# Optimization experiments

Measured on AMD Instinct MI355X. Metric: run time of the kernel, lower is better.

The kernel has to match this reference:

```python
import jax, jax.numpy as jnp
import numpy as np
import math

D_MODEL = 1024
D_STATE = 16
D_CONV = 4
EXPAND = 2
D_INNER = D_MODEL * EXPAND
BATCH = 2
SEQ = 2048


def setup_inputs() -> dict:
    key = jax.random.key(0)
    ks = jax.random.split(key, 8)
    s = 0.02
    x = jax.random.normal(ks[0], (BATCH, SEQ, D_MODEL), dtype=jnp.float32)
    in_proj_w = jax.random.normal(ks[1], (D_MODEL, 2 * D_INNER), dtype=jnp.float32) * s
    conv_w = jax.random.normal(ks[2], (D_INNER, D_CONV), dtype=jnp.float32) * s
    conv_b = jnp.zeros((D_INNER,), dtype=jnp.float32)
    x_proj_w = jax.random.normal(ks[3], (D_INNER, 2 * D_STATE + 1), dtype=jnp.float32) * s
    A_log = jnp.log(jnp.broadcast_to(jnp.arange(1, D_STATE + 1, dtype=jnp.float32)[None, :], (D_INNER, D_STATE)))
    dt_w = jax.random.normal(ks[4], (D_INNER, 1), dtype=jnp.float32) * s
    # special dt bias init: softplus^{-1}(dt_init)
    u = jax.random.uniform(ks[5], (D_INNER,), dtype=jnp.float32)
    dt_init = jnp.exp(u * (math.log(0.1) - math.log(0.001)) + math.log(0.001))
    dt_b = dt_init + jnp.log(-jnp.expm1(-dt_init))
    out_proj_w = jax.random.normal(ks[6], (D_INNER, D_MODEL), dtype=jnp.float32) * s
    ln_g = jnp.ones((D_MODEL,), dtype=jnp.float32)
    ln_b = jnp.zeros((D_MODEL,), dtype=jnp.float32)
    return {"x": x, "in_proj_w": in_proj_w, "conv_w": conv_w, "conv_b": conv_b,
            "x_proj_w": x_proj_w, "A_log": A_log, "dt_w": dt_w, "dt_b": dt_b,
            "out_proj_w": out_proj_w, "ln_g": ln_g, "ln_b": ln_b}


def _silu(x):
    return x * jax.nn.sigmoid(x)


def _layernorm(x, g, b, eps=1e-5):
    mu = jnp.mean(x, axis=-1, keepdims=True)
    var = jnp.mean(jnp.square(x - mu), axis=-1, keepdims=True)
    return (x - mu) * jax.lax.rsqrt(var + eps) * g + b


def _ssm_forward(x, in_proj_w, conv_w, conv_b, x_proj_w, A_log, dt_w, dt_b, out_proj_w, ln_g, ln_b):
    residual = x
    xn = _layernorm(x, ln_g, ln_b)
    xz = xn @ in_proj_w                      # (B, L, 2*d_inner)
    x_b, z = jnp.split(xz, 2, axis=-1)
    # causal depthwise conv1d (pad left d_conv-1, truncate to L)
    xc = jnp.transpose(x_b, (0, 2, 1))       # (B, d_inner, L)
    kern = conv_w[:, None, :]                # (d_inner, 1, K) OIH
    xc = jax.lax.conv_general_dilated(
        xc, kern, window_strides=(1,), padding=[(D_CONV - 1, 0)],
        dimension_numbers=("NCH", "OIH", "NCH"), feature_group_count=D_INNER)
    xc = xc + conv_b[None, :, None]
    x_b = _silu(jnp.transpose(xc, (0, 2, 1)))  # (B, L, d_inner)

    params = x_b @ x_proj_w                  # (B, L, 2*d_state+1)
    B_p = params[:, :, :D_STATE]             # (B, L, d_state)
    C_p = params[:, :, D_STATE:2 * D_STATE]  # (B, L, d_state)
    dt = jax.nn.softplus(params[:, :, -1:] * dt_w[:, 0][None, None, :] + dt_b)  # (B, L, d_inner)
    A = -jnp.exp(A_log)                      # (d_inner, d_state)

    # selective scan over time; per-step dA/dBu computed on the fly
    def step(h, inp):
        u_t, dt_t, B_t, C_t = inp            # (B,di),(B,di),(B,ds),(B,ds)
        dA = jnp.exp(dt_t[..., None] * A)    # (B, d_inner, d_state)
        h = dA * h + (dt_t * u_t)[..., None] * B_t[:, None, :]
        y = jnp.einsum('bds,bs->bd', h, C_t)
        return h, y

    xs = (jnp.swapaxes(x_b, 0, 1), jnp.swapaxes(dt, 0, 1),
          jnp.swapaxes(B_p, 0, 1), jnp.swapaxes(C_p, 0, 1))
    h0 = jnp.zeros((x.shape[0], D_INNER, D_STATE), dtype=x.dtype)
    _, ys = jax.lax.scan(step, h0, xs)       # ys: (L, B, d_inner)
    y = jnp.swapaxes(ys, 0, 1)

    y = y * _silu(z)
    return y @ out_proj_w + residual


def reference(x, in_proj_w, conv_w, conv_b, x_proj_w, A_log, dt_w, dt_b, out_proj_w, ln_g, ln_b):
    return _ssm_forward(x, in_proj_w, conv_w, conv_b, x_proj_w, A_log, dt_w, dt_b, out_proj_w, ln_g, ln_b)
```

## Files before the change

kernel.cpp:

```cpp
#include <hip/hip_runtime.h>
#include <stdint.h>


typedef short short8 __attribute__((ext_vector_type(8)));
typedef float f32x4 __attribute__((ext_vector_type(4)));

#define DEV static __device__ __forceinline__

constexpr int BATCH = 2, SEQ = 2048, DM = 1024, DI = 2048, NST = 16;
constexpr int NTOK = BATCH * SEQ;
constexpr int CH_NC = 32, CH_CL = 64;
constexpr int XP_SLICES = 4, XP_KS = 512;

DEV float bf2f(ushort h) {
    union { uint u; float f; } c; c.u = ((uint)h) << 16; return c.f;
}
DEV ushort f2bf(float x) {
    union { uint u; float f; } c; c.f = x;
    uint u = c.u;
    uint r = (u + 0x7FFFu + ((u >> 16) & 1u)) >> 16;
    return (ushort)r;
}
DEV float softplus_f(float arg) {
    return (arg > 15.f) ? arg : __logf(1.f + __expf(arg));
}
DEV float silu_f(float x) { return x / (1.f + __expf(-x)); }

DEV void stage16(const void* g, void* l) {
    __builtin_amdgcn_global_load_lds(
        (const __attribute__((address_space(1))) void*)g,
        (__attribute__((address_space(3))) void*)l,
        16, 0, 0);
}

__global__ __launch_bounds__(256) void prep_weights(const float* __restrict__ ipw,
                                                    const float* __restrict__ opw,
                                                    const float* __restrict__ xpw,
                                                    ushort* __restrict__ Bt1,
                                                    ushort* __restrict__ Bt2,
                                                    ushort* __restrict__ Wtx) {
    __shared__ float tile[32][33];
    int bid = blockIdx.x;
    int tid = threadIdx.x;
    if (bid < 6144) {
        const float* W; ushort* Bt; int K, N, bx, by;
        if (bid < 4096) { W = ipw; Bt = Bt1; K = 1024; N = 4096; bx = bid & 127; by = bid >> 7; }
        else { int b2 = bid - 4096; W = opw; Bt = Bt2; K = 2048; N = 1024; bx = b2 & 31; by = b2 >> 5; }
        int tx = tid & 31, ty = tid >> 5;
        int n0 = bx * 32, k0 = by * 32;
#pragma unroll
        for (int i = 0; i < 32; i += 8)
            tile[ty + i][tx] = W[(size_t)(k0 + ty + i) * N + n0 + tx];
        __syncthreads();
#pragma unroll
        for (int i = 0; i < 32; i += 8)
            Bt[(size_t)(n0 + ty + i) * K + k0 + tx] = f2bf(tile[tx][ty + i]);
    } else {
        int idx = (bid - 6144) * 256 + tid;
        int j = idx >> 11, k = idx & (DI - 1);
        Wtx[idx] = (j < 33) ? f2bf(xpw[(size_t)k * 33 + j]) : (ushort)0;
    }
}

__global__ __launch_bounds__(256) void ln_kernel(const float* __restrict__ x,
                                                 const float* __restrict__ g,
                                                 const float* __restrict__ b,
                                                 ushort* __restrict__ xn) {
    int row = blockIdx.x;
    int tid = threadIdx.x;
    const float4 v = ((const float4*)(x + (size_t)row * DM))[tid];
    float s = v.x + v.y + v.z + v.w;
    float sq = v.x * v.x + v.y * v.y + v.z * v.z + v.w * v.w;
#pragma unroll
    for (int o = 32; o; o >>= 1) { s += __shfl_down(s, o); sq += __shfl_down(sq, o); }
    __shared__ float ls[4], lsq[4];
    __shared__ float smu, srs;
    int wid = tid >> 6;
    if ((tid & 63) == 0) { ls[wid] = s; lsq[wid] = sq; }
    __syncthreads();
    if (tid == 0) {
        float S = ls[0] + ls[1] + ls[2] + ls[3];
        float SQ = lsq[0] + lsq[1] + lsq[2] + lsq[3];
        float mu = S / DM;
        float var = SQ / DM - mu * mu;
        smu = mu; srs = rsqrtf(var + 1e-5f);
    }
    __syncthreads();
    float mu = smu, rs = srs;
    const float4 gg = ((const float4*)g)[tid];
    const float4 bb = ((const float4*)b)[tid];
    ushort4 o;
    o.x = f2bf((v.x - mu) * rs * gg.x + bb.x);
    o.y = f2bf((v.y - mu) * rs * gg.y + bb.y);
    o.z = f2bf((v.z - mu) * rs * gg.z + bb.z);
    o.w = f2bf((v.w - mu) * rs * gg.w + bb.w);
    ((ushort4*)(xn + (size_t)row * DM))[tid] = o;
}

template <int WM, int WN, int BMW, int BNW, typename OUT_T, bool RES>
__global__ __launch_bounds__(WM * WN * 64, 2) void gemm_pipe(const ushort* __restrict__ A,
                                                             const ushort* __restrict__ Bt,
                                                             OUT_T* __restrict__ C,
                                                             const float* __restrict__ res,
                                                             int M, int N, int K,
                                                             int lda, int ldb) {
    constexpr int THREADS = WM * WN * 64;
    constexpr int BM = WM * BMW * 16, BN = WN * BNW * 16;
    constexpr int CR = THREADS / 8;
    constexpr int NLOADS = (BM + BN) / CR;
    extern __shared__ ushort lds[];

    int tid = threadIdx.x;
    int lane = tid & 63, w = tid >> 6;
    int wm = w / WN, wn = w % WN;
    int lr = lane & 15, kc = lane >> 4;
    int m0 = blockIdx.y * BM, n0 = blockIdx.x * BN;
    int kbase = blockIdx.z * K;
    const ushort* Ag = A + (size_t)m0 * lda + kbase;
    const ushort* Bg = Bt + (size_t)n0 * ldb + kbase;
    C += (size_t)blockIdx.z * M * N;

    int r_in = tid >> 3;
    int sc = (((tid & 7) ^ (r_in & 7))) * 8;
    int lbase_off = 8 * w * 64;

    auto stage = [&](const ushort* gsrc, int ld, ushort* lbase, int nrows, int k0) {
#pragma unroll
        for (int c = 0; c < nrows; c += CR) {
            stage16(gsrc + (size_t)(c + r_in) * ld + k0 + sc,
                    lbase + (size_t)c * 64 + lbase_off);
        }
    };

    f32x4 acc[BMW][BNW];
#pragma unroll
    for (int i = 0; i < BMW; i++)
#pragma unroll
        for (int j = 0; j < BNW; j++) acc[i][j] = (f32x4){0.f, 0.f, 0.f, 0.f};

    const int NT = K >> 6;
    stage(Ag, lda, lds, BM, 0);
    stage(Bg, ldb, lds + BM * 64, BN, 0);

    for (int kt = 0; kt < NT; ++kt) {
        int p = kt & 1;
        ushort* bA = lds + (size_t)p * (BM + BN) * 64;
        ushort* bB = bA + BM * 64;
        ushort* nA = lds + (size_t)(p ^ 1) * (BM + BN) * 64;
        if (kt + 1 < NT) {
            stage(Ag, lda, nA, BM, (kt + 1) * 64);
            stage(Bg, ldb, nA + BM * 64, BN, (kt + 1) * 64);
            if constexpr (NLOADS == 4)
                asm volatile("s_waitcnt vmcnt(4)" ::: "memory");
            else if constexpr (NLOADS == 6)
                asm volatile("s_waitcnt vmcnt(6)" ::: "memory");
            else if constexpr (NLOADS == 8)
                asm volatile("s_waitcnt vmcnt(8)" ::: "memory");
            else
                asm volatile("s_waitcnt vmcnt(0)" ::: "memory");
        } else {
            asm volatile("s_waitcnt vmcnt(0)" ::: "memory");
        }
        __builtin_amdgcn_sched_barrier(0);
        __builtin_amdgcn_s_barrier();
        __builtin_amdgcn_sched_barrier(0);

        short8 bfr[BNW][2];
#pragma unroll
        for (int ni = 0; ni < BNW; ni++)
#pragma unroll
            for (int kk = 0; kk < 2; kk++) {
                int row = wn * BNW * 16 + ni * 16 + lr;
                bfr[ni][kk] = *(const short8*)(bB + (size_t)row * 64 + (((kk * 4 + kc) ^ (lr & 7)) * 8));
            }
        __builtin_amdgcn_s_setprio(1);
#pragma unroll
        for (int mi = 0; mi < BMW; mi++) {
            int row = wm * BMW * 16 + mi * 16 + lr;
            short8 a0 = *(const short8*)(bA + (size_t)row * 64 + (((kc) ^ (lr & 7)) * 8));
            short8 a1 = *(const short8*)(bA + (size_t)row * 64 + (((4 + kc) ^ (lr & 7)) * 8));
#pragma unroll
            for (int ni = 0; ni < BNW; ni++) {
                acc[mi][ni] = __builtin_amdgcn_mfma_f32_16x16x32_bf16(a0, bfr[ni][0], acc[mi][ni], 0, 0, 0);
                acc[mi][ni] = __builtin_amdgcn_mfma_f32_16x16x32_bf16(a1, bfr[ni][1], acc[mi][ni], 0, 0, 0);
            }
        }
        __builtin_amdgcn_s_setprio(0);
        __builtin_amdgcn_sched_barrier(0);
        __builtin_amdgcn_s_barrier();
        __builtin_amdgcn_sched_barrier(0);
    }

#pragma unroll
    for (int mi = 0; mi < BMW; mi++) {
        int r = m0 + wm * BMW * 16 + mi * 16 + kc * 4;
#pragma unroll
        for (int ni = 0; ni < BNW; ni++) {
            int cc = n0 + wn * BNW * 16 + ni * 16 + lr;
#pragma unroll
            for (int j = 0; j < 4; j++) {
                float v = acc[mi][ni][j];
                size_t off = (size_t)(r + j) * N + cc;
                if (RES) v += res[off];
                if constexpr (sizeof(OUT_T) == 2) C[off] = f2bf(v);
                else C[off] = v;
            }
        }
    }
}

__global__ __launch_bounds__(256) void conv_silu(const ushort* __restrict__ xz,
                                                 const float* __restrict__ cw,
                                                 const float* __restrict__ cb,
                                                 ushort* __restrict__ u,
                                                 ushort* __restrict__ szg) {
    int blk = blockIdx.x;
    int b = blk >> 8;
    int t0 = (blk & 255) * 8;
    int d0 = threadIdx.x * 8;

    float4 wreg[8];
#pragma unroll
    for (int j = 0; j < 8; j++) wreg[j] = *(const float4*)(cw + (size_t)(d0 + j) * 4);
    float breg[8];
#pragma unroll
    for (int j = 0; j < 8; j++) breg[j] = cb[d0 + j];

    const short8 zero8 = (short8){0, 0, 0, 0, 0, 0, 0, 0};
    auto loadx = [&](int t) -> short8 {
        if (t < 0) return zero8;
        return *(const short8*)(xz + (size_t)(b * SEQ + t) * (2 * DI) + d0);
    };
    short8 ta = loadx(t0 - 3), tb_ = loadx(t0 - 2), tc = loadx(t0 - 1);
#pragma unroll
    for (int i = 0; i < 8; i++) {
        int row = b * SEQ + t0 + i;
        short8 td = *(const short8*)(xz + (size_t)row * (2 * DI) + d0);
        short8 zv = *(const short8*)(xz + (size_t)row * (2 * DI) + DI + d0);
        short8 u8, sz8;
#pragma unroll
        for (int j = 0; j < 8; j++) {
            float acc = breg[j];
            acc = fmaf(bf2f((ushort)ta[j]), wreg[j].x, acc);
            acc = fmaf(bf2f((ushort)tb_[j]), wreg[j].y, acc);
            acc = fmaf(bf2f((ushort)tc[j]), wreg[j].z, acc);
            acc = fmaf(bf2f((ushort)td[j]), wreg[j].w, acc);
            u8[j] = (short)f2bf(silu_f(acc));
            sz8[j] = (short)f2bf(silu_f(bf2f((ushort)zv[j])));
        }
        *(short8*)(u + (size_t)row * DI + d0) = u8;
        *(short8*)(szg + (size_t)row * DI + d0) = sz8;
        ta = tb_; tb_ = tc; tc = td;
    }
}

__global__ __launch_bounds__(256) void xproj_reduce(const float* __restrict__ part,
                                                    float* __restrict__ params) {
    int i = blockIdx.x * 256 + threadIdx.x;
    const f32x4* p = (const f32x4*)part;
    constexpr size_t SL = (size_t)NTOK * 64 / 4;
    f32x4 s = p[i] + p[SL + i] + p[2 * SL + i] + p[3 * SL + i];
    ((f32x4*)params)[i] = s;
}

DEV void scan_decode(int bid, int tid, int& b, int& chunk, int& d) {
    int lane = tid & 63;
    int w = __builtin_amdgcn_readfirstlane(tid >> 6);
    b = bid >> 8;
    int dg = (bid >> 3) & 31;
    int cq = bid & 7;
    chunk = cq * 4 + w;
    d = dg * 64 + lane;
}

__global__ __launch_bounds__(256) void scan_part1(const ushort* __restrict__ u,
                                                  const float* __restrict__ params,
                                                  const float* __restrict__ A_log,
                                                  const float* __restrict__ dt_w,
                                                  const float* __restrict__ dt_b,
                                                  float* __restrict__ hst,
                                                  float* __restrict__ sdt) {
    int b, chunk, d;
    scan_decode(blockIdx.x, threadIdx.x, b, chunk, d);
    float dtw = dt_w[d], dtbv = dt_b[d];
    float a[16];
#pragma unroll
    for (int s = 0; s < 16; s++) a[s] = -__expf(A_log[(size_t)d * 16 + s]);
    float h[16];
#pragma unroll
    for (int s = 0; s < 16; s++) h[s] = 0.f;
    float sumdt = 0.f;
    int row0 = b * SEQ + chunk * CH_CL;
#pragma unroll 4
    for (int t = 0; t < CH_CL; t++) {
        int row = row0 + t;
        const float* pr = params + (size_t)row * 64;
        float uu = bf2f(u[(size_t)row * DI + d]);
        float dt = softplus_f(fmaf(pr[32], dtw, dtbv));
        sumdt += dt;
        float du = dt * uu;
        const f32x4* Bp = (const f32x4*)pr;
        f32x4 B0 = Bp[0], B1 = Bp[1], B2 = Bp[2], B3 = Bp[3];
#pragma unroll
        for (int r = 0; r < 4; r++) {
            h[r]      = fmaf(h[r],      __expf(dt * a[r]),      du * B0[r]);
            h[4 + r]  = fmaf(h[4 + r],  __expf(dt * a[4 + r]),  du * B1[r]);
            h[8 + r]  = fmaf(h[8 + r],  __expf(dt * a[8 + r]),  du * B2[r]);
            h[12 + r] = fmaf(h[12 + r], __expf(dt * a[12 + r]), du * B3[r]);
        }
    }
    float* hp = hst + (((size_t)(b * CH_NC + chunk) * DI + d) << 4);
#pragma unroll
    for (int s = 0; s < 16; s++) hp[s] = h[s];
    sdt[(size_t)(b * CH_NC + chunk) * DI + d] = sumdt;
}

__global__ __launch_bounds__(256) void scan_stitch(const float* __restrict__ A_log,
                                                   float* __restrict__ hst,
                                                   const float* __restrict__ sdt) {
    int idx = blockIdx.x * 256 + threadIdx.x;
    int s = idx & 15, d = (idx >> 4) & (DI - 1), b = idx >> 15;
    float a = -__expf(A_log[(size_t)d * 16 + s]);
    float carry = 0.f;
    for (int c = 0; c < CH_NC; c++) {
        size_t o = (((size_t)(b * CH_NC + c) * DI + d) << 4) + s;
        float prev = carry;
        carry = fmaf(carry, __expf(a * sdt[(size_t)(b * CH_NC + c) * DI + d]), hst[o]);
        hst[o] = prev;
    }
}

__global__ __launch_bounds__(256) void scan_part2(const ushort* __restrict__ u,
                                                  const float* __restrict__ params,
                                                  const float* __restrict__ A_log,
                                                  const float* __restrict__ dt_w,
                                                  const float* __restrict__ dt_b,
                                                  const float* __restrict__ hst,
                                                  const ushort* __restrict__ szg,
                                                  ushort* __restrict__ yg) {
    int b, chunk, d;
    scan_decode(blockIdx.x, threadIdx.x, b, chunk, d);
    float dtw = dt_w[d], dtbv = dt_b[d];
    float a[16];
#pragma unroll
    for (int s = 0; s < 16; s++) a[s] = -__expf(A_log[(size_t)d * 16 + s]);
    const float* hp = hst + (((size_t)(b * CH_NC + chunk) * DI + d) << 4);
    float h[16];
#pragma unroll
    for (int s = 0; s < 16; s++) h[s] = hp[s];
    int row0 = b * SEQ + chunk * CH_CL;
#pragma unroll 4
    for (int t = 0; t < CH_CL; t++) {
        int row = row0 + t;
        const float* pr = params + (size_t)row * 64;
        float uu = bf2f(u[(size_t)row * DI + d]);
        float dt = softplus_f(fmaf(pr[32], dtw, dtbv));
        float du = dt * uu;
        const f32x4* Bp = (const f32x4*)pr;
        const f32x4* Cp = (const f32x4*)(pr + 16);
        f32x4 B0 = Bp[0], B1 = Bp[1], B2 = Bp[2], B3 = Bp[3];
        f32x4 C0 = Cp[0], C1 = Cp[1], C2 = Cp[2], C3 = Cp[3];
        float y = 0.f;
#pragma unroll
        for (int r = 0; r < 4; r++) {
            h[r]      = fmaf(h[r],      __expf(dt * a[r]),      du * B0[r]);
            h[4 + r]  = fmaf(h[4 + r],  __expf(dt * a[4 + r]),  du * B1[r]);
            h[8 + r]  = fmaf(h[8 + r],  __expf(dt * a[8 + r]),  du * B2[r]);
            h[12 + r] = fmaf(h[12 + r], __expf(dt * a[12 + r]), du * B3[r]);
            y += h[r] * C0[r] + h[4 + r] * C1[r] + h[8 + r] * C2[r] + h[12 + r] * C3[r];
        }
        float sz = bf2f(szg[(size_t)row * DI + d]);
        yg[(size_t)row * DI + d] = f2bf(y * sz);
    }
}

extern "C" void kernel_launch(void* const* d_in, const int* in_sizes, int n_in,
                              void* d_out, int out_size, void* d_ws, size_t ws_size,
                              hipStream_t stream) {
    const float* x    = (const float*)d_in[0];
    const float* ipw  = (const float*)d_in[1];
    const float* cw   = (const float*)d_in[2];
    const float* cb   = (const float*)d_in[3];
    const float* xpw  = (const float*)d_in[4];
    const float* alog = (const float*)d_in[5];
    const float* dtw  = (const float*)d_in[6];
    const float* dtb  = (const float*)d_in[7];
    const float* opw  = (const float*)d_in[8];
    const float* lng  = (const float*)d_in[9];
    const float* lnb  = (const float*)d_in[10];
    float* out = (float*)d_out;

    char* ws = (char*)d_ws;
    size_t off = 0;
    auto carve = [&](size_t bytes) -> void* {
        void* p = ws + off;
        off = (off + bytes + 255) & ~(size_t)255;
        return p;
    };
    ushort* Bt1  = (ushort*)carve((size_t)4096 * 1024 * 2);
    ushort* Bt2  = (ushort*)carve((size_t)1024 * 2048 * 2);
    ushort* Wtx  = (ushort*)carve((size_t)64 * DI * 2);
    ushort* xn   = (ushort*)carve((size_t)NTOK * DM * 2);
    ushort* xz   = (ushort*)carve((size_t)NTOK * 2 * DI * 2);
    ushort* u    = (ushort*)carve((size_t)NTOK * DI * 2);
    ushort* szg  = (ushort*)carve((size_t)NTOK * DI * 2);
    float*  params = (float*)carve((size_t)NTOK * 64 * 4);
    float*  hst  = (float*) carve((size_t)BATCH * CH_NC * DI * NST * 4);
    float*  sdt  = (float*) carve((size_t)BATCH * CH_NC * DI * 4);
    ushort* yg   = (ushort*)carve((size_t)NTOK * DI * 2);
    float*  part = (float*)yg;

    prep_weights<<<6656, 256, 0, stream>>>(ipw, opw, xpw, Bt1, Bt2, Wtx);
    ln_kernel<<<NTOK, 256, 0, stream>>>(x, lng, lnb, xn);
    gemm_pipe<2, 4, 4, 2, ushort, false>
        <<<dim3(32, 32, 1), 512, 2 * (128 + 128) * 64 * sizeof(ushort), stream>>>(
            xn, Bt1, xz, nullptr, NTOK, 4096, 1024, 1024, 1024);
    conv_silu<<<512, 256, 0, stream>>>(xz, cw, cb, u, szg);
    gemm_pipe<2, 2, 2, 2, float, false>
        <<<dim3(1, 64, XP_SLICES), 256, 2 * (64 + 64) * 64 * sizeof(ushort), stream>>>(
            u, Wtx, part, nullptr, NTOK, 64, XP_KS, DI, DI);
    xproj_reduce<<<(NTOK * 64 / 4) / 256, 256, 0, stream>>>(part, params);
    scan_part1<<<512, 256, 0, stream>>>(u, params, alog, dtw, dtb, hst, sdt);
    scan_stitch<<<(BATCH * DI * NST) / 256, 256, 0, stream>>>(alog, hst, sdt);
    scan_part2<<<512, 256, 0, stream>>>(u, params, alog, dtw, dtb, hst, szg, yg);
    gemm_pipe<2, 2, 4, 2, float, true>
        <<<dim3(16, 32, 1), 256, 2 * (128 + 64) * 64 * sizeof(ushort), stream>>>(
            yg, Bt2, out, x, NTOK, 1024, 2048, 2048, 2048);
}
```

Baseline: 180.0 us.

## Split scan state across half-waves, swizzle GEMM blocks, retile GEMMs, use exp2

The selective scan now splits the 16 state dimensions across two half-waves, doubling the block count. Partial outputs are combined with a cross-lane shuffle, and the scan state buffer is laid out state-major for coalesced access. Exponentials use exp2f with A premultiplied by log2(e). The GEMM gains an XCD-aware block-index swizzle, loads all A/B fragments before issuing MFMAs, and in-proj/out-proj switch to 4-wave 128x128 tiles. Together these aim to raise scan parallelism, improve cache locality across dies, and raise per-wave MFMA density, at the cost of more registers per wave and fewer waves in the in-proj GEMM.

```diff
diff --git a/kernel.cpp b/kernel.cpp
--- a/kernel.cpp
+++ b/kernel.cpp
@@ -11,6 +11,7 @@
 constexpr int NTOK = BATCH * SEQ;
 constexpr int CH_NC = 32, CH_CL = 64;
 constexpr int XP_SLICES = 4, XP_KS = 512;
+constexpr float LOG2E = 1.44269504f;
 
 DEV float bf2f(ushort h) {
     union { uint u; float f; } c; c.u = ((uint)h) << 16; return c.f;
@@ -110,11 +111,18 @@
     constexpr int NLOADS = (BM + BN) / CR;
     extern __shared__ ushort lds[];
 
+    int gx = gridDim.x;
+    int nwg = gx * gridDim.y;
+    int lid = blockIdx.y * gx + blockIdx.x;
+    int cpx = nwg >> 3;
+    int swz = (lid & 7) * cpx + (lid >> 3);
+    int bxi = swz % gx, byi = swz / gx;
+
     int tid = threadIdx.x;
     int lane = tid & 63, w = tid >> 6;
     int wm = w / WN, wn = w % WN;
     int lr = lane & 15, kc = lane >> 4;
-    int m0 = blockIdx.y * BM, n0 = blockIdx.x * BN;
+    int m0 = byi * BM, n0 = bxi * BN;
     int kbase = blockIdx.z * K;
     const ushort* Ag = A + (size_t)m0 * lda + kbase;
     const ushort* Bg = Bt + (size_t)n0 * ldb + kbase;
@@ -165,26 +173,29 @@
         __builtin_amdgcn_s_barrier();
         __builtin_amdgcn_sched_barrier(0);
 
-        short8 bfr[BNW][2];
-#pragma unroll
-        for (int ni = 0; ni < BNW; ni++)
-#pragma unroll
-            for (int kk = 0; kk < 2; kk++) {
-                int row = wn * BNW * 16 + ni * 16 + lr;
-                bfr[ni][kk] = *(const short8*)(bB + (size_t)row * 64 + (((kk * 4 + kc) ^ (lr & 7)) * 8));
-            }
-        __builtin_amdgcn_s_setprio(1);
+        short8 af[BMW][2], bfr[BNW][2];
 #pragma unroll
         for (int mi = 0; mi < BMW; mi++) {
             int row = wm * BMW * 16 + mi * 16 + lr;
-            short8 a0 = *(const short8*)(bA + (size_t)row * 64 + (((kc) ^ (lr & 7)) * 8));
-            short8 a1 = *(const short8*)(bA + (size_t)row * 64 + (((4 + kc) ^ (lr & 7)) * 8));
-#pragma unroll
-            for (int ni = 0; ni < BNW; ni++) {
-                acc[mi][ni] = __builtin_amdgcn_mfma_f32_16x16x32_bf16(a0, bfr[ni][0], acc[mi][ni], 0, 0, 0);
-                acc[mi][ni] = __builtin_amdgcn_mfma_f32_16x16x32_bf16(a1, bfr[ni][1], acc[mi][ni], 0, 0, 0);
-            }
-        }
+#pragma unroll
+            for (int kk = 0; kk < 2; kk++)
+                af[mi][kk] = *(const short8*)(bA + (size_t)row * 64 + (((kk * 4 + kc) ^ (lr & 7)) * 8));
+        }
+#pragma unroll
+        for (int ni = 0; ni < BNW; ni++) {
+            int row = wn * BNW * 16 + ni * 16 + lr;
+#pragma unroll
+            for (int kk = 0; kk < 2; kk++)
+                bfr[ni][kk] = *(const short8*)(bB + (size_t)row * 64 + (((kk * 4 + kc) ^ (lr & 7)) * 8));
+        }
+        __builtin_amdgcn_s_setprio(1);
+#pragma unroll
+        for (int kk = 0; kk < 2; kk++)
+#pragma unroll
+            for (int mi = 0; mi < BMW; mi++)
+#pragma unroll
+                for (int ni = 0; ni < BNW; ni++)
+                    acc[mi][ni] = __builtin_amdgcn_mfma_f32_16x16x32_bf16(af[mi][kk], bfr[ni][kk], acc[mi][ni], 0, 0, 0);
         __builtin_amdgcn_s_setprio(0);
         __builtin_amdgcn_sched_barrier(0);
         __builtin_amdgcn_s_barrier();
@@ -263,14 +274,15 @@
     ((f32x4*)params)[i] = s;
 }
 
-DEV void scan_decode(int bid, int tid, int& b, int& chunk, int& d) {
+DEV void scan_decode(int bid, int tid, int& b, int& chunk, int& d, int& sh) {
     int lane = tid & 63;
-    int w = __builtin_amdgcn_readfirstlane(tid >> 6);
-    b = bid >> 8;
-    int dg = (bid >> 3) & 31;
+    int w = tid >> 6;
+    b = bid >> 9;
+    int dg = (bid >> 3) & 63;
     int cq = bid & 7;
     chunk = cq * 4 + w;
-    d = dg * 64 + lane;
+    d = dg * 32 + (lane & 31);
+    sh = lane >> 5;
 }
 
 __global__ __launch_bounds__(256) void scan_part1(const ushort* __restrict__ u,
@@ -280,15 +292,16 @@
                                                   const float* __restrict__ dt_b,
                                                   float* __restrict__ hst,
                                                   float* __restrict__ sdt) {
-    int b, chunk, d;
-    scan_decode(blockIdx.x, threadIdx.x, b, chunk, d);
+    int b, chunk, d, sh;
+    scan_decode(blockIdx.x, threadIdx.x, b, chunk, d, sh);
     float dtw = dt_w[d], dtbv = dt_b[d];
-    float a[16];
-#pragma unroll
-    for (int s = 0; s < 16; s++) a[s] = -__expf(A_log[(size_t)d * 16 + s]);
-    float h[16];
-#pragma unroll
-    for (int s = 0; s < 16; s++) h[s] = 0.f;
+    float a2[8];
+#pragma unroll
+    for (int s = 0; s < 8; s++)
+        a2[s] = -__expf(A_log[(size_t)d * 16 + sh * 8 + s]) * LOG2E;
+    float h[8];
+#pragma unroll
+    for (int s = 0; s < 8; s++) h[s] = 0.f;
     float sumdt = 0.f;
     int row0 = b * SEQ + chunk * CH_CL;
 #pragma unroll 4
@@ -299,33 +312,33 @@
         float dt = softplus_f(fmaf(pr[32], dtw, dtbv));
         sumdt += dt;
         float du = dt * uu;
-        const f32x4* Bp = (const f32x4*)pr;
-        f32x4 B0 = Bp[0], B1 = Bp[1], B2 = Bp[2], B3 = Bp[3];
+        const f32x4* Bp = (const f32x4*)(pr + sh * 8);
+        f32x4 B0 = Bp[0], B1 = Bp[1];
 #pragma unroll
         for (int r = 0; r < 4; r++) {
-            h[r]      = fmaf(h[r],      __expf(dt * a[r]),      du * B0[r]);
-            h[4 + r]  = fmaf(h[4 + r],  __expf(dt * a[4 + r]),  du * B1[r]);
-            h[8 + r]  = fmaf(h[8 + r],  __expf(dt * a[8 + r]),  du * B2[r]);
-            h[12 + r] = fmaf(h[12 + r], __expf(dt * a[12 + r]), du * B3[r]);
-        }
-    }
-    float* hp = hst + (((size_t)(b * CH_NC + chunk) * DI + d) << 4);
-#pragma unroll
-    for (int s = 0; s < 16; s++) hp[s] = h[s];
-    sdt[(size_t)(b * CH_NC + chunk) * DI + d] = sumdt;
+            h[r]     = fmaf(h[r],     exp2f(dt * a2[r]),     du * B0[r]);
+            h[4 + r] = fmaf(h[4 + r], exp2f(dt * a2[4 + r]), du * B1[r]);
+        }
+    }
+    size_t base = ((size_t)(b * CH_NC + chunk) * 16 + sh * 8) * DI + d;
+#pragma unroll
+    for (int s = 0; s < 8; s++) hst[base + (size_t)s * DI] = h[s];
+    if (sh == 0) sdt[(size_t)(b * CH_NC + chunk) * DI + d] = sumdt;
 }
 
 __global__ __launch_bounds__(256) void scan_stitch(const float* __restrict__ A_log,
                                                    float* __restrict__ hst,
                                                    const float* __restrict__ sdt) {
     int idx = blockIdx.x * 256 + threadIdx.x;
-    int s = idx & 15, d = (idx >> 4) & (DI - 1), b = idx >> 15;
-    float a = -__expf(A_log[(size_t)d * 16 + s]);
+    int d = idx & (DI - 1);
+    int s = (idx >> 11) & 15;
+    int b = idx >> 15;
+    float a2 = -__expf(A_log[(size_t)d * 16 + s]) * LOG2E;
     float carry = 0.f;
     for (int c = 0; c < CH_NC; c++) {
-        size_t o = (((size_t)(b * CH_NC + c) * DI + d) << 4) + s;
+        size_t o = ((size_t)(b * CH_NC + c) * 16 + s) * DI + d;
         float prev = carry;
-        carry = fmaf(carry, __expf(a * sdt[(size_t)(b * CH_NC + c) * DI + d]), hst[o]);
+        carry = fmaf(carry, exp2f(a2 * sdt[(size_t)(b * CH_NC + c) * DI + d]), hst[o]);
         hst[o] = prev;
     }
 }
@@ -338,16 +351,17 @@
                                                   const float* __restrict__ hst,
                                                   const ushort* __restrict__ szg,
                                                   ushort* __restrict__ yg) {
-    int b, chunk, d;
-    scan_decode(blockIdx.x, threadIdx.x, b, chunk, d);
+    int b, chunk, d, sh;
+    scan_decode(blockIdx.x, threadIdx.x, b, chunk, d, sh);
     float dtw = dt_w[d], dtbv = dt_b[d];
-    float a[16];
-#pragma unroll
-    for (int s = 0; s < 16; s++) a[s] = -__expf(A_log[(size_t)d * 16 + s]);
-    const float* hp = hst + (((size_t)(b * CH_NC + chunk) * DI + d) << 4);
-    float h[16];
-#pragma unroll
-    for (int s = 0; s < 16; s++) h[s] = hp[s];
+    float a2[8];
+#pragma unroll
+    for (int s = 0; s < 8; s++)
+        a2[s] = -__expf(A_log[(size_t)d * 16 + sh * 8 + s]) * LOG2E;
+    size_t base = ((size_t)(b * CH_NC + chunk) * 16 + sh * 8) * DI + d;
+    float h[8];
+#pragma unroll
+    for (int s = 0; s < 8; s++) h[s] = hst[base + (size_t)s * DI];
     int row0 = b * SEQ + chunk * CH_CL;
 #pragma unroll 4
     for (int t = 0; t < CH_CL; t++) {
@@ -356,21 +370,22 @@
         float uu = bf2f(u[(size_t)row * DI + d]);
         float dt = softplus_f(fmaf(pr[32], dtw, dtbv));
         float du = dt * uu;
-        const f32x4* Bp = (const f32x4*)pr;
-        const f32x4* Cp = (const f32x4*)(pr + 16);
-        f32x4 B0 = Bp[0], B1 = Bp[1], B2 = Bp[2], B3 = Bp[3];
-        f32x4 C0 = Cp[0], C1 = Cp[1], C2 = Cp[2], C3 = Cp[3];
+        const f32x4* Bp = (const f32x4*)(pr + sh * 8);
+        const f32x4* Cp = (const f32x4*)(pr + 16 + sh * 8);
+        f32x4 B0 = Bp[0], B1 = Bp[1];
+        f32x4 C0 = Cp[0], C1 = Cp[1];
         float y = 0.f;
 #pragma unroll
         for (int r = 0; r < 4; r++) {
-            h[r]      = fmaf(h[r],      __expf(dt * a[r]),      du * B0[r]);
-            h[4 + r]  = fmaf(h[4 + r],  __expf(dt * a[4 + r]),  du * B1[r]);
-            h[8 + r]  = fmaf(h[8 + r],  __expf(dt * a[8 + r]),  du * B2[r]);
-            h[12 + r] = fmaf(h[12 + r], __expf(dt * a[12 + r]), du * B3[r]);
-            y += h[r] * C0[r] + h[4 + r] * C1[r] + h[8 + r] * C2[r] + h[12 + r] * C3[r];
-        }
-        float sz = bf2f(szg[(size_t)row * DI + d]);
-        yg[(size_t)row * DI + d] = f2bf(y * sz);
+            h[r]     = fmaf(h[r],     exp2f(dt * a2[r]),     du * B0[r]);
+            h[4 + r] = fmaf(h[4 + r], exp2f(dt * a2[4 + r]), du * B1[r]);
+            y += h[r] * C0[r] + h[4 + r] * C1[r];
+        }
+        y += __shfl_xor(y, 32);
+        if (sh == 0) {
+            float sz = bf2f(szg[(size_t)row * DI + d]);
+            yg[(size_t)row * DI + d] = f2bf(y * sz);
+        }
     }
 }
 
@@ -405,25 +420,25 @@
     ushort* u    = (ushort*)carve((size_t)NTOK * DI * 2);
     ushort* szg  = (ushort*)carve((size_t)NTOK * DI * 2);
     float*  params = (float*)carve((size_t)NTOK * 64 * 4);
-    float*  hst  = (float*) carve((size_t)BATCH * CH_NC * DI * NST * 4);
+    float*  hst  = (float*) carve((size_t)BATCH * CH_NC * NST * DI * 4);
     float*  sdt  = (float*) carve((size_t)BATCH * CH_NC * DI * 4);
     ushort* yg   = (ushort*)carve((size_t)NTOK * DI * 2);
     float*  part = (float*)yg;
 
     prep_weights<<<6656, 256, 0, stream>>>(ipw, opw, xpw, Bt1, Bt2, Wtx);
     ln_kernel<<<NTOK, 256, 0, stream>>>(x, lng, lnb, xn);
-    gemm_pipe<2, 4, 4, 2, ushort, false>
-        <<<dim3(32, 32, 1), 512, 2 * (128 + 128) * 64 * sizeof(ushort), stream>>>(
+    gemm_pipe<2, 2, 4, 4, ushort, false>
+        <<<dim3(32, 32, 1), 256, 2 * (128 + 128) * 64 * sizeof(ushort), stream>>>(
             xn, Bt1, xz, nullptr, NTOK, 4096, 1024, 1024, 1024);
     conv_silu<<<512, 256, 0, stream>>>(xz, cw, cb, u, szg);
     gemm_pipe<2, 2, 2, 2, float, false>
         <<<dim3(1, 64, XP_SLICES), 256, 2 * (64 + 64) * 64 * sizeof(ushort), stream>>>(
             u, Wtx, part, nullptr, NTOK, 64, XP_KS, DI, DI);
     xproj_reduce<<<(NTOK * 64 / 4) / 256, 256, 0, stream>>>(part, params);
-    scan_part1<<<512, 256, 0, stream>>>(u, params, alog, dtw, dtb, hst, sdt);
+    scan_part1<<<1024, 256, 0, stream>>>(u, params, alog, dtw, dtb, hst, sdt);
     scan_stitch<<<(BATCH * DI * NST) / 256, 256, 0, stream>>>(alog, hst, sdt);
-    scan_part2<<<512, 256, 0, stream>>>(u, params, alog, dtw, dtb, hst, szg, yg);
-    gemm_pipe<2, 2, 4, 2, float, true>
-        <<<dim3(16, 32, 1), 256, 2 * (128 + 64) * 64 * sizeof(ushort), stream>>>(
+    scan_part2<<<1024, 256, 0, stream>>>(u, params, alog, dtw, dtb, hst, szg, yg);
+    gemm_pipe<2, 2, 4, 4, float, true>
+        <<<dim3(8, 32, 1), 256, 2 * (128 + 128) * 64 * sizeof(ushort), stream>>>(
             yg, Bt2, out, x, NTOK, 1024, 2048, 2048, 2048);
 }
```

Result: slower. 236.5 us (+31.4%).
